# Performance work log

Hardware: AMD Instinct MI355X
Metric: run time of the kernel (lower is better)

Reference implementation:

```python
import jax, jax.numpy as jnp
import numpy as np

BEV_H, BEV_W = 496, 432  # cfg.bevshape

def mish(x):
    return x * jnp.tanh(jax.nn.softplus(x))

def ln(x, g, b, eps=1e-5):
    m = jnp.mean(x, axis=-1, keepdims=True)
    v = jnp.mean((x - m) ** 2, axis=-1, keepdims=True)
    return (x - m) * jax.lax.rsqrt(v + eps) * g + b

def fel(x, W, g, b):
    # FELayer: Linear(bias=False) -> LayerNorm -> Mish
    return mish(ln(x @ W.T, g, b))

def setup_inputs() -> dict:
    key = jax.random.key(0)
    ks = iter(jax.random.split(key, 48))
    Nv, P, Cin, Cv, Nb = 16000, 32, 10, 64, 16000
    inp = {}
    inp['voxels'] = jax.random.normal(next(ks), (Nv, P, Cin), jnp.float32)
    inp['voxelmask'] = jax.random.bernoulli(next(ks), 0.7, (Nv, P, 1)).astype(jnp.float32)
    inp['bevsidx'] = jax.random.randint(next(ks), (Nb, 64), 0, Nv, dtype=jnp.int32)
    flat = jax.random.choice(next(ks), BEV_H * BEV_W, (Nb,), replace=False)
    inp['bevcoors'] = jnp.stack([flat // BEV_W, flat % BEV_W], axis=1).astype(jnp.int32)
    inp['bevmask'] = jax.random.bernoulli(next(ks), 0.8, (Nb, 1, 1)).astype(jnp.float32)
    def w(shape):
        return jax.random.normal(next(ks), shape, jnp.float32) * 0.05
    for i, cin in zip((1, 2, 3, 4), (Cin, Cv, Cv, Cv)):
        inp[f'vfe{i}_W'] = w((Cv, cin))
        inp[f'vfe{i}_g'] = jnp.ones((Cv,), jnp.float32)
        inp[f'vfe{i}_b'] = jnp.zeros((Cv,), jnp.float32)
    inp['bfe1_W'] = w((16, Cv, Cv));  inp['bfe1_g'] = jnp.ones((16, Cv));  inp['bfe1_b'] = jnp.zeros((16, Cv))
    inp['bfe2a_W'] = w((16, 8, Cv)); inp['bfe2a_g'] = jnp.ones((16, 8));  inp['bfe2a_b'] = jnp.zeros((16, 8))
    inp['bfe2b_W'] = w((16, 8, 32)); inp['bfe2b_g'] = jnp.ones((16, 8));  inp['bfe2b_b'] = jnp.zeros((16, 8))
    inp['bfe3_W'] = w((128, 128));   inp['bfe3_g'] = jnp.ones((128,));   inp['bfe3_b'] = jnp.zeros((128,))
    return inp

def reference(voxels, voxelmask, bevsidx, bevcoors, bevmask,
              vfe1_W, vfe1_g, vfe1_b, vfe2_W, vfe2_g, vfe2_b,
              vfe3_W, vfe3_g, vfe3_b, vfe4_W, vfe4_g, vfe4_b,
              bfe1_W, bfe1_g, bfe1_b, bfe2a_W, bfe2a_g, bfe2a_b,
              bfe2b_W, bfe2b_g, bfe2b_b, bfe3_W, bfe3_g, bfe3_b):
    # voxel feature encoder with masked residual
    x1 = fel(voxels, vfe1_W, vfe1_g, vfe1_b)            # [Nv, P, 64]
    x2 = fel(x1, vfe2_W, vfe2_g, vfe2_b) * voxelmask
    x3 = fel(x2, vfe3_W, vfe3_g, vfe3_b)
    x4 = fel(x3, vfe4_W, vfe4_g, vfe4_b) * voxelmask + x2
    voxelwise = jnp.max(x4, axis=1)                     # [Nv, 64]
    # gather 64 voxels per BEV cell
    bevs = voxelwise[bevsidx]                           # [Nb, 64 voxels, 64 ch]
    x0 = jnp.transpose(bevs, (0, 2, 1))                 # [Nb, 64 ch, 64 voxels]
    Nb = x0.shape[0]
    xg = x0.reshape(Nb, 16, 4, 64)                      # 16 branches of 4 channel-rows
    # bfe1_k (vectorized over the 16 branches) + bev mask
    h = mish(ln(jnp.einsum('ngpc,goc->ngpo', xg, bfe1_W), bfe1_g[:, None, :], bfe1_b[:, None, :]))
    h = h * bevmask[:, None]                            # bevmask [Nb,1,1] -> broadcast
    # bfe2_k: NormalFELayer(in_points=4, in=64, out=8)
    h = mish(ln(jnp.einsum('ngpc,goc->ngpo', h, bfe2a_W), bfe2a_g[:, None, :], bfe2a_b[:, None, :]))
    h = h.reshape(Nb, 16, 32)
    h = mish(ln(jnp.einsum('ngc,goc->ngo', h, bfe2b_W), bfe2b_g, bfe2b_b))  # [Nb,16,8]
    x17 = h.reshape(Nb, 128)                            # cat of 16 branches
    x18 = fel(x17, bfe3_W, bfe3_g, bfe3_b)
    x19 = fel(x18, bfe3_W, bfe3_g, bfe3_b) + x17        # same bfe3 applied twice + residual
    bevmap = jnp.zeros((BEV_H, BEV_W, 128), jnp.float32).at[bevcoors[:, 0], bevcoors[:, 1]].set(x19)
    return jnp.transpose(bevmap, (2, 1, 0))             # [128, W, H]
```

## Files before the change

kernel.cpp:

```cpp
#include <hip/hip_runtime.h>
#include <math.h>

constexpr int NV  = 16000;
constexpr int P   = 32;
constexpr int CIN = 10;
constexpr int CV  = 64;
constexpr int NB  = 16000;
constexpr int BEV_H = 496, BEV_W = 432;
constexpr int HW = BEV_H * BEV_W;
constexpr float EPS = 1e-5f;

typedef __attribute__((ext_vector_type(8))) short short8_t;
typedef __attribute__((ext_vector_type(4))) short short4_t;
typedef __attribute__((ext_vector_type(4))) float fx4;
typedef __attribute__((ext_vector_type(2))) float f32x2;

__device__ __forceinline__ float mish(float x) {
  float e = __expf(fminf(x, 15.f));
  float u = 1.f + e;
  float d = fmaf(u, u, 1.f);
  float r = __builtin_amdgcn_rcpf(d);
  return fmaf(-2.f * x, r, x);
}

__device__ __forceinline__ short f2bf(float f) {
  unsigned u = __builtin_bit_cast(unsigned, f);
  u += 0x7FFF + ((u >> 16) & 1);
  return (short)(u >> 16);
}
__device__ __forceinline__ float bf2f(short s) {
  unsigned u = ((unsigned)(unsigned short)s) << 16;
  return __builtin_bit_cast(float, u);
}
__device__ __forceinline__ short8_t pack8(const float* t) {
  short8_t s;
#pragma unroll
  for (int j = 0; j < 8; ++j) s[j] = f2bf(t[j]);
  return s;
}

__device__ __forceinline__ unsigned bfpair(float a, float b) {
  unsigned au = __builtin_bit_cast(unsigned, a) + 0x8000u;
  unsigned bu = __builtin_bit_cast(unsigned, b) + 0x8000u;
  return __builtin_amdgcn_perm(bu, au, 0x07060302u);
}
__device__ __forceinline__ unsigned hipack(float a, float b, float& la, float& lb) {
  unsigned ua = (__builtin_bit_cast(unsigned, a) + 0x8000u) & 0xFFFF0000u;
  unsigned ub = (__builtin_bit_cast(unsigned, b) + 0x8000u) & 0xFFFF0000u;
  la = a - __builtin_bit_cast(float, ua);
  lb = b - __builtin_bit_cast(float, ub);
  return __builtin_amdgcn_perm(ub, ua, 0x07060302u);
}

__global__ __launch_bounds__(256) void pack_weights_kernel(
    const float* __restrict__ W1, const float* __restrict__ W2a,
    const float* __restrict__ W2b, const float* __restrict__ W3,
    short* __restrict__ w1h,
    short* __restrict__ w2ah,
    short* __restrict__ w2bh,
    short* __restrict__ w3h, short* __restrict__ w3l)
{
  int i = blockIdx.x * 256 + threadIdx.x;
  if (i < 65536) {
    w1h[i] = f2bf(W1[i]);
  } else if (i < 81920) {
    int j = i - 65536;
    int g = j >> 10, o = (j >> 6) & 15, c = j & 63;
    float v = (o < 8) ? W2a[(g * 8 + o) * 64 + c] : 0.f;
    w2ah[j] = f2bf(v);
  } else if (i < 90112) {
    int k = i - 81920;
    int g = k >> 9, o = (k >> 5) & 15, c = k & 31;
    float v = (o < 8) ? W2b[(g * 8 + o) * 32 + c] : 0.f;
    w2bh[k] = f2bf(v);
  } else if (i < 106496) {
    int j = i - 90112;
    float v = W3[j];
    short h = f2bf(v);
    w3h[j] = h; w3l[j] = f2bf(v - bf2f(h));
  }
}

__global__ __launch_bounds__(256, 4) void vfe_mfma5_kernel(
    const float* __restrict__ voxels, const float* __restrict__ vmask,
    const float* __restrict__ W1, const float* __restrict__ g1, const float* __restrict__ b1,
    const float* __restrict__ W2, const float* __restrict__ g2, const float* __restrict__ b2,
    const float* __restrict__ W3, const float* __restrict__ g3, const float* __restrict__ b3,
    const float* __restrict__ W4, const float* __restrict__ g4, const float* __restrict__ b4,
    unsigned short* __restrict__ voxelwise)
{
  __shared__ short wlds[28 * 512];
  __shared__ short actb[4][16 * 72];
  __shared__ float gblds[512];

  const int tid  = threadIdx.x;
  const int lane = tid & 63;
  const int w    = tid >> 6;
  const int p    = lane & 15;
  const int q    = lane >> 4;
  const int gw   = blockIdx.x * 4 + w;

  for (int k = tid; k < 512; k += 256) {
    int region = k >> 6, off = k & 63;
    const float* src =
        region == 0 ? g1 : region == 1 ? b1 :
        region == 2 ? g2 : region == 3 ? b2 :
        region == 4 ? g3 : region == 5 ? b3 :
        region == 6 ? g4 : b4;
    gblds[k] = src[off];
  }
  for (int s = w; s < 28; s += 4) {
    float t[8];
    if (s < 4) {
      const int f = s;
#pragma unroll
      for (int j = 0; j < 8; ++j) {
        int c = 8 * q + j;
        t[j] = (c < CIN) ? W1[(p + 16 * f) * CIN + c] : 0.f;
      }
    } else {
      const int l = (s - 4) >> 3, rem = (s - 4) & 7, ch = rem >> 2, f = rem & 3;
      const float* Wl = (l == 0) ? W2 : (l == 1) ? W3 : W4;
      const float* src = Wl + (p + 16 * f) * CV + 32 * ch + 8 * q;
#pragma unroll
      for (int j = 0; j < 8; ++j) t[j] = src[j];
    }
    *(short8_t*)&wlds[s * 512 + lane * 8] = pack8(t);
  }
  __syncthreads();

  short* mybuf = &actb[w][0];
  const fx4 zacc = {0.f, 0.f, 0.f, 0.f};
  const int srcLane = ((lane >> 2) & 3) * 16 + (((lane >> 4) & 3) << 2) + (lane & 3);

  for (int i = 0; i < 4; ++i) {
    const int v = gw * 4 + i;
    float chmax0 = 0.f, vmaxv = 0.f;

    for (int h = 0; h < 2; ++h) {
      const int ptbase = v * 32 + h * 16;
      const float m = vmask[ptbase + p];
      float x2r[16];
      float cur[16];

      {
        const float* xrow = voxels + (size_t)(ptbase + p) * CIN;
        float t[8] = {0.f, 0.f, 0.f, 0.f, 0.f, 0.f, 0.f, 0.f};
        if (q == 0) {
          float2 a = *(const float2*)(xrow + 0);
          float2 b = *(const float2*)(xrow + 2);
          float2 c = *(const float2*)(xrow + 4);
          float2 d = *(const float2*)(xrow + 6);
          t[0] = a.x; t[1] = a.y; t[2] = b.x; t[3] = b.y;
          t[4] = c.x; t[5] = c.y; t[6] = d.x; t[7] = d.y;
        } else if (q == 1) {
          float2 a = *(const float2*)(xrow + 8);
          t[0] = a.x; t[1] = a.y;
        }
        uint4 bu = make_uint4(bfpair(t[0], t[1]), bfpair(t[2], t[3]),
                              bfpair(t[4], t[5]), bfpair(t[6], t[7]));
        short8_t bfrag = __builtin_bit_cast(short8_t, bu);
        fx4 acc[4];
#pragma unroll
        for (int f = 0; f < 4; ++f) {
          short8_t af = *(short8_t*)&wlds[f * 512 + lane * 8];
          acc[f] = __builtin_amdgcn_mfma_f32_16x16x32_bf16(af, bfrag, zacc, 0, 0, 0);
        }
        f32x2 s1v = {0.f, 0.f}, s2v = {0.f, 0.f};
#pragma unroll
        for (int f = 0; f < 4; ++f) {
          f32x2 a01 = __builtin_shufflevector(acc[f], acc[f], 0, 1);
          f32x2 a23 = __builtin_shufflevector(acc[f], acc[f], 2, 3);
          s1v = s1v + a01 + a23;
          s2v = __builtin_elementwise_fma(a01, a01, s2v);
          s2v = __builtin_elementwise_fma(a23, a23, s2v);
        }
        float s1 = s1v[0] + s1v[1], s2 = s2v[0] + s2v[1];
        s1 += __shfl_xor(s1, 16); s1 += __shfl_xor(s1, 32);
        s2 += __shfl_xor(s2, 16); s2 += __shfl_xor(s2, 32);
        float mean = s1 * (1.f / 64.f);
        float rstd = rsqrtf(fmaf(-mean, mean, s2 * (1.f / 64.f)) + EPS);
        float ms = -mean * rstd;
#pragma unroll
        for (int f = 0; f < 4; ++f) {
          float4 gv = *(const float4*)&gblds[16 * f + 4 * q];
          float4 bv = *(const float4*)&gblds[64 + 16 * f + 4 * q];
          float go[4] = {gv.x, gv.y, gv.z, gv.w};
          float bo[4] = {bv.x, bv.y, bv.z, bv.w};
          float o[4];
#pragma unroll
          for (int r = 0; r < 4; ++r)
            o[r] = mish(fmaf(fmaf(acc[f][r], rstd, ms), go[r], bo[r]));
          *(uint2*)&mybuf[p * 72 + 4 * q + 16 * f] =
              make_uint2(bfpair(o[0], o[1]), bfpair(o[2], o[3]));
        }
      }

#pragma unroll 1
      for (int l = 0; l < 3; ++l) {
        short8_t bf0 = *(short8_t*)&mybuf[p * 72 + 8 * q];
        short8_t bf1 = *(short8_t*)&mybuf[p * 72 + 8 * q + 32];
        fx4 acc[4];
#pragma unroll
        for (int f = 0; f < 4; ++f) {
          short8_t a0 = *(short8_t*)&wlds[(4 + l * 8 + f) * 512 + lane * 8];
          short8_t a1 = *(short8_t*)&wlds[(4 + l * 8 + 4 + f) * 512 + lane * 8];
          fx4 a = __builtin_amdgcn_mfma_f32_16x16x32_bf16(a0, bf0, zacc, 0, 0, 0);
          acc[f] = __builtin_amdgcn_mfma_f32_16x16x32_bf16(a1, bf1, a, 0, 0, 0);
        }
        f32x2 s1v = {0.f, 0.f}, s2v = {0.f, 0.f};
#pragma unroll
        for (int f = 0; f < 4; ++f) {
          f32x2 a01 = __builtin_shufflevector(acc[f], acc[f], 0, 1);
          f32x2 a23 = __builtin_shufflevector(acc[f], acc[f], 2, 3);
          s1v = s1v + a01 + a23;
          s2v = __builtin_elementwise_fma(a01, a01, s2v);
          s2v = __builtin_elementwise_fma(a23, a23, s2v);
        }
        float s1 = s1v[0] + s1v[1], s2 = s2v[0] + s2v[1];
        s1 += __shfl_xor(s1, 16); s1 += __shfl_xor(s1, 32);
        s2 += __shfl_xor(s2, 16); s2 += __shfl_xor(s2, 32);
        float mean = s1 * (1.f / 64.f);
        float rstd = rsqrtf(fmaf(-mean, mean, s2 * (1.f / 64.f)) + EPS);
        float ms = -mean * rstd;
        const int gbbase = (l + 1) * 128;
#pragma unroll
        for (int f = 0; f < 4; ++f) {
          float4 gv = *(const float4*)&gblds[gbbase + 16 * f + 4 * q];
          float4 bv = *(const float4*)&gblds[gbbase + 64 + 16 * f + 4 * q];
          float go[4] = {gv.x, gv.y, gv.z, gv.w};
          float bo[4] = {bv.x, bv.y, bv.z, bv.w};
          if (l == 0) {
            float o[4];
#pragma unroll
            for (int r = 0; r < 4; ++r) {
              o[r] = mish(fmaf(fmaf(acc[f][r], rstd, ms), go[r], bo[r])) * m;
              x2r[f * 4 + r] = o[r];
            }
            *(uint2*)&mybuf[p * 72 + 4 * q + 16 * f] =
                make_uint2(bfpair(o[0], o[1]), bfpair(o[2], o[3]));
          } else if (l == 1) {
            float o[4];
#pragma unroll
            for (int r = 0; r < 4; ++r)
              o[r] = mish(fmaf(fmaf(acc[f][r], rstd, ms), go[r], bo[r]));
            *(uint2*)&mybuf[p * 72 + 4 * q + 16 * f] =
                make_uint2(bfpair(o[0], o[1]), bfpair(o[2], o[3]));
          } else {
#pragma unroll
            for (int r = 0; r < 4; ++r) {
              float t1 = fmaf(fmaf(acc[f][r], rstd, ms), go[r], bo[r]);
              cur[f * 4 + r] = fmaf(mish(t1), m, x2r[f * 4 + r]);
            }
          }
        }
      }

#pragma unroll
      for (int t = 0; t < 8; ++t) {
        float send = (lane & 8) ? cur[t] : cur[t + 8];
        float got  = __shfl_xor(send, 8);
        float mine = (lane & 8) ? cur[t + 8] : cur[t];
        cur[t] = fmaxf(mine, got);
      }
#pragma unroll
      for (int t = 0; t < 4; ++t) {
        float send = (lane & 4) ? cur[t] : cur[t + 4];
        float got  = __shfl_xor(send, 4);
        float mine = (lane & 4) ? cur[t + 4] : cur[t];
        cur[t] = fmaxf(mine, got);
      }
#pragma unroll
      for (int t = 0; t < 2; ++t) {
        float send = (lane & 2) ? cur[t] : cur[t + 2];
        float got  = __shfl_xor(send, 2);
        float mine = (lane & 2) ? cur[t + 2] : cur[t];
        cur[t] = fmaxf(mine, got);
      }
      {
        float send = (lane & 1) ? cur[0] : cur[1];
        float got  = __shfl_xor(send, 1);
        float mine = (lane & 1) ? cur[1] : cur[0];
        cur[0] = fmaxf(mine, got);
      }
      float hm = __shfl(cur[0], srcLane);
      if (h == 0) chmax0 = hm; else vmaxv = fmaxf(chmax0, hm);
    }
    unsigned uv = __builtin_bit_cast(unsigned, vmaxv) + 0x8000u;
    voxelwise[v * 64 + lane] = (unsigned short)(uv >> 16);
  }
}

constexpr int XS_CH   = 72;
constexpr int XS_CELL = 16 * 72 + 16;
constexpr int ACT_OFF = 8 * XS_CELL;
constexpr int ACT_WS  = 16 * 72;
constexpr int H2_OFF  = ACT_OFF + 4 * ACT_WS;
constexpr int H2_WS   = 16 * 40;
constexpr int X17_OFF = H2_OFF + 4 * H2_WS;
constexpr int SMEM_SHORTS = X17_OFF + 8 * 132 * 2;

__global__ __launch_bounds__(256, 4) void bfe12_mfma4_kernel(
    const unsigned short* __restrict__ voxelwise, const int* __restrict__ bevsidx,
    const float* __restrict__ bevmask,
    const short* __restrict__ w1h,
    const float* __restrict__ g1, const float* __restrict__ b1,
    const short* __restrict__ w2ah,
    const float* __restrict__ g2a, const float* __restrict__ b2a,
    const short* __restrict__ w2bh,
    const float* __restrict__ g2b, const float* __restrict__ b2b,
    float* __restrict__ x17buf)
{
  extern __shared__ short sm[];
  float* x17lds = (float*)&sm[X17_OFF];

  const int tid  = threadIdx.x;
  const int lane = tid & 63;
  const int w    = tid >> 6;
  const int r15  = lane & 15;
  const int q    = lane >> 4;
  const int cellbase = blockIdx.x * 8;

  const int chq   = lane & 3;
  const int v_loc = (lane >> 2) & 3;
  const int vblk  = lane >> 4;
  const int bit0  = v_loc & 1, bit1 = v_loc >> 1;

  int idxr[2][4];
#pragma unroll
  for (int cc = 0; cc < 2; ++cc)
#pragma unroll
    for (int vb = 0; vb < 4; ++vb) {
      int v = 16 * vb + 4 * vblk + v_loc;
      idxr[cc][vb] = bevsidx[(cellbase + 2 * w + cc) * 64 + v];
    }

  {
    short* zh = &sm[H2_OFF + w * H2_WS];
    for (int i = lane; i < 320; i += 64) zh[320 + i] = 0;
  }

  const fx4 zacc = {0.f, 0.f, 0.f, 0.f};
  short* acth = &sm[ACT_OFF + w * ACT_WS];
  short* h2h  = &sm[H2_OFF + w * H2_WS];

#pragma unroll 1
  for (int j = 0; j < 4; ++j) {
    const int g = 4 * j + w;

    __syncthreads();

#pragma unroll
    for (int cc = 0; cc < 2; ++cc) {
#pragma unroll
      for (int vb = 0; vb < 4; ++vb) {
        const unsigned short* src =
            voxelwise + (size_t)idxr[cc][vb] * 64 + 16 * j + 4 * chq;
        uint2 u2 = *(const uint2*)src;
        float a0 = __builtin_bit_cast(float, u2.x << 16);
        float a1 = __builtin_bit_cast(float, u2.x & 0xFFFF0000u);
        float a2 = __builtin_bit_cast(float, u2.y << 16);
        float a3 = __builtin_bit_cast(float, u2.y & 0xFFFF0000u);
        float gv0 = bit0 ? a0 : a1, gv1 = bit0 ? a2 : a3;
        float r0 = __shfl_xor(gv0, 4), r1 = __shfl_xor(gv1, 4);
        float c0 = bit0 ? r0 : a0, c1 = bit0 ? a1 : r0;
        float c2 = bit0 ? r1 : a2, c3 = bit0 ? a3 : r1;
        float h0 = bit1 ? c0 : c2, h1 = bit1 ? c1 : c3;
        float s0 = __shfl_xor(h0, 8), s1 = __shfl_xor(h1, 8);
        float d0 = bit1 ? s0 : c0, d1 = bit1 ? s1 : c1;
        float d2 = bit1 ? c2 : s0, d3 = bit1 ? c3 : s1;
        int addr = (2 * w + cc) * XS_CELL + (4 * chq + v_loc) * XS_CH + 16 * vb + 4 * vblk;
        *(uint2*)&sm[addr] = make_uint2(bfpair(d0, d1), bfpair(d2, d3));
      }
    }

    __syncthreads();

    short8_t W1f[2][4];
#pragma unroll
    for (int c = 0; c < 2; ++c)
#pragma unroll
      for (int f = 0; f < 4; ++f) {
        int off = (g * 64 + r15 + 16 * f) * 64 + 32 * c + 8 * q;
        W1f[c][f] = *(const short8_t*)&w1h[off];
      }
    short8_t W2af[2];
#pragma unroll
    for (int c = 0; c < 2; ++c) {
      int off = (g * 16 + r15) * 64 + 32 * c + 8 * q;
      W2af[c] = *(const short8_t*)&w2ah[off];
    }
    short8_t W2bf;
    {
      int off = (g * 16 + r15) * 32 + 8 * q;
      W2bf = *(const short8_t*)&w2bh[off];
    }

#pragma unroll 1
    for (int t = 0; t < 2; ++t) {
      const int cl = r15 >> 2, p = r15 & 3;
      const int cell_loc = 4 * t + cl;
      const float bm = bevmask[cellbase + cell_loc];

      int xaddr = cell_loc * XS_CELL + (4 * w + p) * XS_CH;
      short8_t x0 = *(short8_t*)&sm[xaddr + 8 * q];
      short8_t x1 = *(short8_t*)&sm[xaddr + 32 + 8 * q];

      fx4 acc[4];
#pragma unroll
      for (int f = 0; f < 4; ++f) {
        fx4 a = __builtin_amdgcn_mfma_f32_16x16x32_bf16(W1f[0][f], x0, zacc, 0, 0, 0);
        acc[f] = __builtin_amdgcn_mfma_f32_16x16x32_bf16(W1f[1][f], x1, a, 0, 0, 0);
      }

      f32x2 s1v = {0.f, 0.f}, s2v = {0.f, 0.f};
#pragma unroll
      for (int f = 0; f < 4; ++f) {
        f32x2 a01 = __builtin_shufflevector(acc[f], acc[f], 0, 1);
        f32x2 a23 = __builtin_shufflevector(acc[f], acc[f], 2, 3);
        s1v = s1v + a01 + a23;
        s2v = __builtin_elementwise_fma(a01, a01, s2v);
        s2v = __builtin_elementwise_fma(a23, a23, s2v);
      }
      float s1 = s1v[0] + s1v[1], s2 = s2v[0] + s2v[1];
      s1 += __shfl_xor(s1, 16); s1 += __shfl_xor(s1, 32);
      s2 += __shfl_xor(s2, 16); s2 += __shfl_xor(s2, 32);
      float mean = s1 * (1.f / 64.f);
      float rstd = rsqrtf(fmaf(-mean, mean, s2 * (1.f / 64.f)) + EPS);
      float ms = -mean * rstd;

#pragma unroll
      for (int f = 0; f < 4; ++f) {
        float4 gv = *(const float4*)(g1 + g * 64 + 16 * f + 4 * q);
        float4 bv = *(const float4*)(b1 + g * 64 + 16 * f + 4 * q);
        float go[4] = {gv.x, gv.y, gv.z, gv.w};
        float bo[4] = {bv.x, bv.y, bv.z, bv.w};
        float o[4];
#pragma unroll
        for (int r = 0; r < 4; ++r)
          o[r] = mish(fmaf(fmaf(acc[f][r], rstd, ms), go[r], bo[r])) * bm;
        *(uint2*)&acth[r15 * 72 + 16 * f + 4 * q] =
            make_uint2(bfpair(o[0], o[1]), bfpair(o[2], o[3]));
      }

      short8_t a0 = *(short8_t*)&acth[r15 * 72 + 8 * q];
      short8_t a1 = *(short8_t*)&acth[r15 * 72 + 32 + 8 * q];
      fx4 a2 = __builtin_amdgcn_mfma_f32_16x16x32_bf16(W2af[0], a0, zacc, 0, 0, 0);
      a2 = __builtin_amdgcn_mfma_f32_16x16x32_bf16(W2af[1], a1, a2, 0, 0, 0);

      float sa = a2[0] + a2[1] + a2[2] + a2[3];
      float sb = fmaf(a2[0], a2[0], fmaf(a2[1], a2[1], fmaf(a2[2], a2[2], a2[3] * a2[3])));
      sa += __shfl_xor(sa, 16); sb += __shfl_xor(sb, 16);
      if (q < 2) {
        float mean2 = sa * 0.125f;
        float rstd2 = rsqrtf(fmaf(-mean2, mean2, sb * 0.125f) + EPS);
        float ms2 = -mean2 * rstd2;
        float4 gv = *(const float4*)(g2a + g * 8 + 4 * q);
        float4 bv = *(const float4*)(b2a + g * 8 + 4 * q);
        float go[4] = {gv.x, gv.y, gv.z, gv.w};
        float bo[4] = {bv.x, bv.y, bv.z, bv.w};
        float o[4];
#pragma unroll
        for (int r = 0; r < 4; ++r)
          o[r] = mish(fmaf(fmaf(a2[r], rstd2, ms2), go[r], bo[r]));
        *(uint2*)&h2h[cell_loc * 40 + p * 8 + 4 * q] =
            make_uint2(bfpair(o[0], o[1]), bfpair(o[2], o[3]));
      }
    }

    {
      short8_t bh = *(short8_t*)&h2h[r15 * 40 + 8 * q];
      fx4 a3 = __builtin_amdgcn_mfma_f32_16x16x32_bf16(W2bf, bh, zacc, 0, 0, 0);

      float sa = a3[0] + a3[1] + a3[2] + a3[3];
      float sb = fmaf(a3[0], a3[0], fmaf(a3[1], a3[1], fmaf(a3[2], a3[2], a3[3] * a3[3])));
      sa += __shfl_xor(sa, 16); sb += __shfl_xor(sb, 16);
      if (q < 2 && r15 < 8) {
        float mean3 = sa * 0.125f;
        float rstd3 = rsqrtf(fmaf(-mean3, mean3, sb * 0.125f) + EPS);
        float ms3 = -mean3 * rstd3;
        float4 gv = *(const float4*)(g2b + g * 8 + 4 * q);
        float4 bv = *(const float4*)(b2b + g * 8 + 4 * q);
        float go[4] = {gv.x, gv.y, gv.z, gv.w};
        float bo[4] = {bv.x, bv.y, bv.z, bv.w};
        float4 outv;
        float* op = &outv.x;
#pragma unroll
        for (int r = 0; r < 4; ++r)
          op[r] = mish(fmaf(fmaf(a3[r], rstd3, ms3), go[r], bo[r]));
        *(float4*)&x17lds[r15 * 132 + g * 8 + 4 * q] = outv;
      }
    }
  }

  __syncthreads();
  {
    const int cell = tid >> 5;
    const int off  = (tid & 31) * 4;
    float4 vq = *(const float4*)&x17lds[cell * 132 + off];
    *(float4*)&x17buf[(size_t)(cellbase + cell) * 128 + off] = vq;
  }
}

__global__ __launch_bounds__(256, 3) void bfe3_mfma2_kernel(
    const float* __restrict__ x17buf, const int* __restrict__ bevcoors,
    const short* __restrict__ w3h, const short* __restrict__ w3l,
    const float* __restrict__ g3, const float* __restrict__ b3,
    float* __restrict__ out)
{
  __shared__ short x18h[4][16 * 136];
  __shared__ short x18l[4][16 * 136];

  const int tid  = threadIdx.x;
  const int lane = tid & 63;
  const int w    = tid >> 6;
  const int r15  = lane & 15;
  const int q    = lane >> 4;
  const int cell = blockIdx.x * 64 + w * 16 + r15;
  const float* xr = x17buf + (size_t)cell * 128;
  short* xh18 = &x18h[w][0];
  short* xl18 = &x18l[w][0];
  const fx4 zacc = {0.f, 0.f, 0.f, 0.f};

  short8_t xh[4], xl[4];
#pragma unroll
  for (int c = 0; c < 4; ++c) {
    const float* s = xr + 32 * c + 8 * q;
    float4 A = *(const float4*)s;
    float4 B = *(const float4*)(s + 4);
    float t[8] = {A.x, A.y, A.z, A.w, B.x, B.y, B.z, B.w};
    unsigned hu[4], lu[4];
#pragma unroll
    for (int jj = 0; jj < 4; ++jj) {
      float la, lb;
      hu[jj] = hipack(t[2 * jj], t[2 * jj + 1], la, lb);
      lu[jj] = bfpair(la, lb);
    }
    xh[c] = __builtin_bit_cast(short8_t, make_uint4(hu[0], hu[1], hu[2], hu[3]));
    xl[c] = __builtin_bit_cast(short8_t, make_uint4(lu[0], lu[1], lu[2], lu[3]));
  }

  fx4 acc[8];
#pragma unroll
  for (int f = 0; f < 8; ++f) {
    fx4 a = zacc;
#pragma unroll
    for (int c = 0; c < 4; ++c) {
      int off = (16 * f + r15) * 128 + 32 * c + 8 * q;
      short8_t Ah = *(const short8_t*)&w3h[off];
      short8_t Al = *(const short8_t*)&w3l[off];
      a = __builtin_amdgcn_mfma_f32_16x16x32_bf16(Ah, xh[c], a, 0, 0, 0);
      a = __builtin_amdgcn_mfma_f32_16x16x32_bf16(Ah, xl[c], a, 0, 0, 0);
      a = __builtin_amdgcn_mfma_f32_16x16x32_bf16(Al, xh[c], a, 0, 0, 0);
    }
    acc[f] = a;
  }
  {
    f32x2 s1v = {0.f, 0.f}, s2v = {0.f, 0.f};
#pragma unroll
    for (int f = 0; f < 8; ++f) {
      f32x2 a01 = __builtin_shufflevector(acc[f], acc[f], 0, 1);
      f32x2 a23 = __builtin_shufflevector(acc[f], acc[f], 2, 3);
      s1v = s1v + a01 + a23;
      s2v = __builtin_elementwise_fma(a01, a01, s2v);
      s2v = __builtin_elementwise_fma(a23, a23, s2v);
    }
    float s1 = s1v[0] + s1v[1], s2 = s2v[0] + s2v[1];
    s1 += __shfl_xor(s1, 16); s1 += __shfl_xor(s1, 32);
    s2 += __shfl_xor(s2, 16); s2 += __shfl_xor(s2, 32);
    float mean = s1 * (1.f / 128.f);
    float rstd = rsqrtf(fmaf(-mean, mean, s2 * (1.f / 128.f)) + EPS);
    float ms = -mean * rstd;
#pragma unroll
    for (int f = 0; f < 8; ++f) {
      float4 gv = *(const float4*)(g3 + 16 * f + 4 * q);
      float4 bv = *(const float4*)(b3 + 16 * f + 4 * q);
      float go[4] = {gv.x, gv.y, gv.z, gv.w};
      float bo[4] = {bv.x, bv.y, bv.z, bv.w};
      float o[4];
#pragma unroll
      for (int r = 0; r < 4; ++r)
        o[r] = mish(fmaf(fmaf(acc[f][r], rstd, ms), go[r], bo[r]));
      float la0, lb0, la1, lb1;
      unsigned h01 = hipack(o[0], o[1], la0, lb0);
      unsigned h23 = hipack(o[2], o[3], la1, lb1);
      *(uint2*)&xh18[r15 * 136 + 16 * f + 4 * q] = make_uint2(h01, h23);
      *(uint2*)&xl18[r15 * 136 + 16 * f + 4 * q] =
          make_uint2(bfpair(la0, lb0), bfpair(la1, lb1));
    }
  }

  short8_t yh[4], yl[4];
#pragma unroll
  for (int c = 0; c < 4; ++c) {
    yh[c] = *(short8_t*)&xh18[r15 * 136 + 32 * c + 8 * q];
    yl[c] = *(short8_t*)&xl18[r15 * 136 + 32 * c + 8 * q];
  }
#pragma unroll
  for (int f = 0; f < 8; ++f) {
    fx4 a = zacc;
#pragma unroll
    for (int c = 0; c < 4; ++c) {
      int off = (16 * f + r15) * 128 + 32 * c + 8 * q;
      short8_t Ah = *(const short8_t*)&w3h[off];
      short8_t Al = *(const short8_t*)&w3l[off];
      a = __builtin_amdgcn_mfma_f32_16x16x32_bf16(Ah, yh[c], a, 0, 0, 0);
      a = __builtin_amdgcn_mfma_f32_16x16x32_bf16(Ah, yl[c], a, 0, 0, 0);
      a = __builtin_amdgcn_mfma_f32_16x16x32_bf16(Al, yh[c], a, 0, 0, 0);
    }
    acc[f] = a;
  }
  {
    f32x2 s1v = {0.f, 0.f}, s2v = {0.f, 0.f};
#pragma unroll
    for (int f = 0; f < 8; ++f) {
      f32x2 a01 = __builtin_shufflevector(acc[f], acc[f], 0, 1);
      f32x2 a23 = __builtin_shufflevector(acc[f], acc[f], 2, 3);
      s1v = s1v + a01 + a23;
      s2v = __builtin_elementwise_fma(a01, a01, s2v);
      s2v = __builtin_elementwise_fma(a23, a23, s2v);
    }
    float s1 = s1v[0] + s1v[1], s2 = s2v[0] + s2v[1];
    s1 += __shfl_xor(s1, 16); s1 += __shfl_xor(s1, 32);
    s2 += __shfl_xor(s2, 16); s2 += __shfl_xor(s2, 32);
    float mean = s1 * (1.f / 128.f);
    float rstd = rsqrtf(fmaf(-mean, mean, s2 * (1.f / 128.f)) + EPS);
    float ms = -mean * rstd;

    int2 hw2 = *(const int2*)&bevcoors[cell * 2];
    const int base = hw2.y * BEV_H + hw2.x;
#pragma unroll
    for (int f = 0; f < 8; ++f) {
      float4 gv = *(const float4*)(g3 + 16 * f + 4 * q);
      float4 bv = *(const float4*)(b3 + 16 * f + 4 * q);
      float go[4] = {gv.x, gv.y, gv.z, gv.w};
      float bo[4] = {bv.x, bv.y, bv.z, bv.w};
      float4 R = *(const float4*)(xr + 16 * f + 4 * q);
      float Ra[4] = {R.x, R.y, R.z, R.w};
#pragma unroll
      for (int r = 0; r < 4; ++r) {
        float t1 = fmaf(fmaf(acc[f][r], rstd, ms), go[r], bo[r]);
        float val = mish(t1) + Ra[r];
        out[(size_t)(16 * f + 4 * q + r) * HW + base] = val;
      }
    }
  }
}

extern "C" void kernel_launch(void* const* d_in, const int* in_sizes, int n_in,
                              void* d_out, int out_size, void* d_ws, size_t ws_size,
                              hipStream_t stream) {
  const float* voxels   = (const float*)d_in[0];
  const float* vmask    = (const float*)d_in[1];
  const int*   bevsidx  = (const int*)d_in[2];
  const int*   bevcoors = (const int*)d_in[3];
  const float* bevmask  = (const float*)d_in[4];
  const float* vfe1_W = (const float*)d_in[5];
  const float* vfe1_g = (const float*)d_in[6];
  const float* vfe1_b = (const float*)d_in[7];
  const float* vfe2_W = (const float*)d_in[8];
  const float* vfe2_g = (const float*)d_in[9];
  const float* vfe2_b = (const float*)d_in[10];
  const float* vfe3_W = (const float*)d_in[11];
  const float* vfe3_g = (const float*)d_in[12];
  const float* vfe3_b = (const float*)d_in[13];
  const float* vfe4_W = (const float*)d_in[14];
  const float* vfe4_g = (const float*)d_in[15];
  const float* vfe4_b = (const float*)d_in[16];
  const float* bfe1_W  = (const float*)d_in[17];
  const float* bfe1_g  = (const float*)d_in[18];
  const float* bfe1_b  = (const float*)d_in[19];
  const float* bfe2a_W = (const float*)d_in[20];
  const float* bfe2a_g = (const float*)d_in[21];
  const float* bfe2a_b = (const float*)d_in[22];
  const float* bfe2b_W = (const float*)d_in[23];
  const float* bfe2b_g = (const float*)d_in[24];
  const float* bfe2b_b = (const float*)d_in[25];
  const float* bfe3_W  = (const float*)d_in[26];
  const float* bfe3_g  = (const float*)d_in[27];
  const float* bfe3_b  = (const float*)d_in[28];

  unsigned short* voxelwise = (unsigned short*)d_ws;
  float* x17buf = (float*)(voxelwise + (size_t)NV * 64);
  short* wbase  = (short*)(x17buf + (size_t)NB * 128);
  short* w1h  = wbase;
  short* w2ah = w1h + 65536;
  short* w2bh = w2ah + 16384;
  short* w3h  = w2bh + 8192;
  short* w3l  = w3h + 16384;
  float* out = (float*)d_out;

  hipMemsetAsync(d_out, 0, (size_t)out_size * sizeof(float), stream);

  pack_weights_kernel<<<(106496 + 255) / 256, 256, 0, stream>>>(
      bfe1_W, bfe2a_W, bfe2b_W, bfe3_W,
      w1h, w2ah, w2bh, w3h, w3l);

  vfe_mfma5_kernel<<<NV / 16, 256, 0, stream>>>(
      voxels, vmask,
      vfe1_W, vfe1_g, vfe1_b, vfe2_W, vfe2_g, vfe2_b,
      vfe3_W, vfe3_g, vfe3_b, vfe4_W, vfe4_g, vfe4_b,
      voxelwise);

  bfe12_mfma4_kernel<<<NB / 8, 256, SMEM_SHORTS * sizeof(short), stream>>>(
      voxelwise, bevsidx, bevmask,
      w1h, bfe1_g, bfe1_b,
      w2ah, bfe2a_g, bfe2a_b,
      w2bh, bfe2b_g, bfe2b_b,
      x17buf);

  bfe3_mfma2_kernel<<<NB / 64, 256, 0, stream>>>(
      x17buf, bevcoors, w3h, w3l, bfe3_g, bfe3_b, out);
}
```

Baseline: 433.4 us.

## Gather all voxel channels upfront per cell and drop per-branch-group barriers

```diff
diff --git a/kernel.cpp b/kernel.cpp
--- a/kernel.cpp
+++ b/kernel.cpp
@@ -292,15 +292,31 @@
 }
 
 constexpr int XS_CH   = 72;
-constexpr int XS_CELL = 16 * 72 + 16;
-constexpr int ACT_OFF = 8 * XS_CELL;
+constexpr int XS_CELL = 64 * 72 + 16;
+constexpr int ACT_OFF = 4 * XS_CELL;
 constexpr int ACT_WS  = 16 * 72;
 constexpr int H2_OFF  = ACT_OFF + 4 * ACT_WS;
 constexpr int H2_WS   = 16 * 40;
 constexpr int X17_OFF = H2_OFF + 4 * H2_WS;
-constexpr int SMEM_SHORTS = X17_OFF + 8 * 132 * 2;
-
-__global__ __launch_bounds__(256, 4) void bfe12_mfma4_kernel(
+constexpr int SMEM_SHORTS = X17_OFF + 4 * 132 * 2;
+
+__device__ __forceinline__ uint2 gather_transpose(uint2 u2, int bit0, int bit1) {
+  float a0 = __builtin_bit_cast(float, u2.x << 16);
+  float a1 = __builtin_bit_cast(float, u2.x & 0xFFFF0000u);
+  float a2 = __builtin_bit_cast(float, u2.y << 16);
+  float a3 = __builtin_bit_cast(float, u2.y & 0xFFFF0000u);
+  float gv0 = bit0 ? a0 : a1, gv1 = bit0 ? a2 : a3;
+  float r0 = __shfl_xor(gv0, 4), r1 = __shfl_xor(gv1, 4);
+  float c0 = bit0 ? r0 : a0, c1 = bit0 ? a1 : r0;
+  float c2 = bit0 ? r1 : a2, c3 = bit0 ? a3 : r1;
+  float h0 = bit1 ? c0 : c2, h1 = bit1 ? c1 : c3;
+  float s0 = __shfl_xor(h0, 8), s1 = __shfl_xor(h1, 8);
+  float d0 = bit1 ? s0 : c0, d1 = bit1 ? s1 : c1;
+  float d2 = bit1 ? c2 : s0, d3 = bit1 ? c3 : s1;
+  return make_uint2(bfpair(d0, d1), bfpair(d2, d3));
+}
+
+__global__ __launch_bounds__(256, 3) void bfe12_mfma6_kernel(
     const unsigned short* __restrict__ voxelwise, const int* __restrict__ bevsidx,
     const float* __restrict__ bevmask,
     const short* __restrict__ w1h,
@@ -319,26 +335,41 @@
   const int w    = tid >> 6;
   const int r15  = lane & 15;
   const int q    = lane >> 4;
-  const int cellbase = blockIdx.x * 8;
+  const int cellbase = blockIdx.x * 4;
 
   const int chq   = lane & 3;
   const int v_loc = (lane >> 2) & 3;
   const int vblk  = lane >> 4;
   const int bit0  = v_loc & 1, bit1 = v_loc >> 1;
 
-  int idxr[2][4];
-#pragma unroll
-  for (int cc = 0; cc < 2; ++cc)
-#pragma unroll
-    for (int vb = 0; vb < 4; ++vb) {
-      int v = 16 * vb + 4 * vblk + v_loc;
-      idxr[cc][vb] = bevsidx[(cellbase + 2 * w + cc) * 64 + v];
-    }
+  int idxr[4];
+#pragma unroll
+  for (int vb = 0; vb < 4; ++vb)
+    idxr[vb] = bevsidx[(cellbase + w) * 64 + 16 * vb + 4 * vblk + v_loc];
 
   {
     short* zh = &sm[H2_OFF + w * H2_WS];
-    for (int i = lane; i < 320; i += 64) zh[320 + i] = 0;
-  }
+    for (int i = lane; i < 480; i += 64) zh[160 + i] = 0;
+  }
+
+  uint2 raw[4][4];
+#pragma unroll
+  for (int vb = 0; vb < 4; ++vb)
+#pragma unroll
+    for (int js = 0; js < 4; ++js)
+      raw[vb][js] = *(const uint2*)(voxelwise + (size_t)idxr[vb] * 64 +
+                                    16 * js + 4 * chq);
+#pragma unroll
+  for (int js = 0; js < 4; ++js)
+#pragma unroll
+    for (int vb = 0; vb < 4; ++vb) {
+      uint2 packed = gather_transpose(raw[vb][js], bit0, bit1);
+      int addr = w * XS_CELL + (16 * js + 4 * chq + v_loc) * XS_CH +
+                 16 * vb + 4 * vblk;
+      *(uint2*)&sm[addr] = packed;
+    }
+
+  __syncthreads();
 
   const fx4 zacc = {0.f, 0.f, 0.f, 0.f};
   short* acth = &sm[ACT_OFF + w * ACT_WS];
@@ -347,34 +378,6 @@
 #pragma unroll 1
   for (int j = 0; j < 4; ++j) {
     const int g = 4 * j + w;
-
-    __syncthreads();
-
-#pragma unroll
-    for (int cc = 0; cc < 2; ++cc) {
-#pragma unroll
-      for (int vb = 0; vb < 4; ++vb) {
-        const unsigned short* src =
-            voxelwise + (size_t)idxr[cc][vb] * 64 + 16 * j + 4 * chq;
-        uint2 u2 = *(const uint2*)src;
-        float a0 = __builtin_bit_cast(float, u2.x << 16);
-        float a1 = __builtin_bit_cast(float, u2.x & 0xFFFF0000u);
-        float a2 = __builtin_bit_cast(float, u2.y << 16);
-        float a3 = __builtin_bit_cast(float, u2.y & 0xFFFF0000u);
-        float gv0 = bit0 ? a0 : a1, gv1 = bit0 ? a2 : a3;
-        float r0 = __shfl_xor(gv0, 4), r1 = __shfl_xor(gv1, 4);
-        float c0 = bit0 ? r0 : a0, c1 = bit0 ? a1 : r0;
-        float c2 = bit0 ? r1 : a2, c3 = bit0 ? a3 : r1;
-        float h0 = bit1 ? c0 : c2, h1 = bit1 ? c1 : c3;
-        float s0 = __shfl_xor(h0, 8), s1 = __shfl_xor(h1, 8);
-        float d0 = bit1 ? s0 : c0, d1 = bit1 ? s1 : c1;
-        float d2 = bit1 ? c2 : s0, d3 = bit1 ? c3 : s1;
-        int addr = (2 * w + cc) * XS_CELL + (4 * chq + v_loc) * XS_CH + 16 * vb + 4 * vblk;
-        *(uint2*)&sm[addr] = make_uint2(bfpair(d0, d1), bfpair(d2, d3));
-      }
-    }
-
-    __syncthreads();
 
     short8_t W1f[2][4];
 #pragma unroll
@@ -396,13 +399,11 @@
       W2bf = *(const short8_t*)&w2bh[off];
     }
 
-#pragma unroll 1
-    for (int t = 0; t < 2; ++t) {
+    {
       const int cl = r15 >> 2, p = r15 & 3;
-      const int cell_loc = 4 * t + cl;
-      const float bm = bevmask[cellbase + cell_loc];
-
-      int xaddr = cell_loc * XS_CELL + (4 * w + p) * XS_CH;
+      const float bm = bevmask[cellbase + cl];
+
+      int xaddr = cl * XS_CELL + (4 * g + p) * XS_CH;
       short8_t x0 = *(short8_t*)&sm[xaddr + 8 * q];
       short8_t x1 = *(short8_t*)&sm[xaddr + 32 + 8 * q];
 
@@ -463,7 +464,7 @@
 #pragma unroll
         for (int r = 0; r < 4; ++r)
           o[r] = mish(fmaf(fmaf(a2[r], rstd2, ms2), go[r], bo[r]));
-        *(uint2*)&h2h[cell_loc * 40 + p * 8 + 4 * q] =
+        *(uint2*)&h2h[cl * 40 + p * 8 + 4 * q] =
             make_uint2(bfpair(o[0], o[1]), bfpair(o[2], o[3]));
       }
     }
@@ -475,7 +476,7 @@
       float sa = a3[0] + a3[1] + a3[2] + a3[3];
       float sb = fmaf(a3[0], a3[0], fmaf(a3[1], a3[1], fmaf(a3[2], a3[2], a3[3] * a3[3])));
       sa += __shfl_xor(sa, 16); sb += __shfl_xor(sb, 16);
-      if (q < 2 && r15 < 8) {
+      if (q < 2 && r15 < 4) {
         float mean3 = sa * 0.125f;
         float rstd3 = rsqrtf(fmaf(-mean3, mean3, sb * 0.125f) + EPS);
         float ms3 = -mean3 * rstd3;
@@ -494,7 +495,7 @@
   }
 
   __syncthreads();
-  {
+  if (tid < 128) {
     const int cell = tid >> 5;
     const int off  = (tid & 31) * 4;
     float4 vq = *(const float4*)&x17lds[cell * 132 + off];
@@ -702,7 +703,7 @@
       vfe3_W, vfe3_g, vfe3_b, vfe4_W, vfe4_g, vfe4_b,
       voxelwise);
 
-  bfe12_mfma4_kernel<<<NB / 8, 256, SMEM_SHORTS * sizeof(short), stream>>>(
+  bfe12_mfma6_kernel<<<NB / 4, 256, SMEM_SHORTS * sizeof(short), stream>>>(
       voxelwise, bevsidx, bevmask,
       w1h, bfe1_g, bfe1_b,
       w2ah, bfe2a_g, bfe2a_b,
```

Result: no change. 426.1 us (-1.7%).
